# Performance work log

Measured on AMD Instinct MI355X. Metric: run time of the kernel, lower is better.

Reference implementation:

```python
import jax, jax.numpy as jnp
import numpy as np

EPS = 1e-5

def layernorm(x, w, b):
    mu = jnp.mean(x, axis=-1, keepdims=True)
    var = jnp.mean((x - mu) ** 2, axis=-1, keepdims=True)
    return (x - mu) / jnp.sqrt(var + EPS) * w + b

def setup_inputs() -> dict:
    key = jax.random.key(0)
    ks = jax.random.split(key, 20)
    N, E, G = 50000, 800000, 512
    IN, OUT, TXT, MAN = 128, 128, 768, 14
    d = {
        "x": jax.random.normal(ks[0], (N, IN), jnp.float32),
        "edge_index": jax.random.randint(ks[1], (2, E), 0, N),
        "batch": jnp.sort(jax.random.randint(ks[2], (N,), 0, G)),
        "batch_size": G,
        "text_embedding": jax.random.normal(ks[3], (G, TXT), jnp.float32),
        "features_embedding": jax.random.normal(ks[4], (G, MAN), jnp.float32),
        # params
        "ln_proj_w": jnp.ones((IN,)), "ln_proj_b": jnp.zeros((IN,)),
        "W_l": jax.random.normal(ks[5], (IN, OUT)) / np.sqrt(IN),
        "b_l": jnp.zeros((OUT,)),
        "W_r": jax.random.normal(ks[6], (IN, OUT)) / np.sqrt(IN),
        "ln_conv_w": jnp.ones((OUT,)), "ln_conv_b": jnp.zeros((OUT,)),
        "gate_w": jax.random.normal(ks[7], (OUT, 1)) / np.sqrt(OUT),
        "gate_b": jnp.zeros((1,)),
        "graph_weight": jnp.asarray(1.0, jnp.float32),
        "msg_W": jax.random.normal(ks[8], (TXT, OUT)) / np.sqrt(TXT),
        "msg_b": jnp.zeros((OUT,)),
        "feat_W": jax.random.normal(ks[9], (MAN, OUT)) / np.sqrt(MAN),
        "feat_b": jnp.zeros((OUT,)),
        "mixed_w": jnp.ones((3 * OUT,)), "mixed_b": jnp.zeros((3 * OUT,)),
        "fc1_W": jax.random.normal(ks[10], (3 * OUT, 1)) / np.sqrt(3 * OUT),
        "fc1_b": jnp.zeros((1,)),
    }
    return d

def reference(x, edge_index, batch, batch_size, text_embedding, features_embedding,
              ln_proj_w, ln_proj_b, W_l, b_l, W_r, ln_conv_w, ln_conv_b,
              gate_w, gate_b, graph_weight, msg_W, msg_b, feat_W, feat_b,
              mixed_w, mixed_b, fc1_W, fc1_b):
    N = x.shape[0]
    src, dst = edge_index[0], edge_index[1]
    # project_norm
    h = layernorm(x, ln_proj_w, ln_proj_b)
    # GraphSAGE (SAGEConv, mean aggregation): out = mean_j(h_j) @ W_l + b + h @ W_r
    msgs = h[src]                                   # [E, IN] gather
    agg = jax.ops.segment_sum(msgs, dst, num_segments=N)
    deg = jax.ops.segment_sum(jnp.ones((src.shape[0],), h.dtype), dst, num_segments=N)
    mean_nb = agg / jnp.maximum(deg, 1.0)[:, None]
    h = mean_nb @ W_l + b_l + h @ W_r
    # layernorm + gelu (HomogeneousGraphConvolution)
    h = jax.nn.gelu(layernorm(h, ln_conv_w, ln_conv_b), approximate=False)
    # AttentionalAggregation: scatter-softmax over `batch`
    gate = (h @ gate_w + gate_b)[:, 0]              # [N]
    seg_max = jax.ops.segment_max(gate, batch, num_segments=batch_size)
    seg_max = jnp.where(jnp.isfinite(seg_max), seg_max, 0.0)
    e = jnp.exp(gate - seg_max[batch])
    denom = jax.ops.segment_sum(e, batch, num_segments=batch_size)
    attn = (e / denom[batch])[:, None]              # [N,1]
    graph_embedding = jax.ops.segment_sum(attn * h, batch, num_segments=batch_size)
    # dropout is identity in eval mode
    weighted = graph_weight * graph_embedding
    msg_emb = jax.nn.gelu(text_embedding @ msg_W + msg_b, approximate=False)
    feat_emb = jax.nn.gelu(features_embedding @ feat_W + feat_b, approximate=False)
    emb = jnp.concatenate([weighted, msg_emb, feat_emb], axis=1)
    emb = layernorm(emb, mixed_w, mixed_b)
    logits = emb @ fc1_W + fc1_b
    return (logits, graph_embedding, attn)
```

## Files before the change

kernel.cpp:

```cpp
#include <hip/hip_runtime.h>


typedef unsigned short ushort_t;
typedef __attribute__((ext_vector_type(8))) short bf16x8;
typedef __attribute__((ext_vector_type(4))) float floatx4;

#define NBLK 128
#define MAXNB 1024

__device__ __forceinline__ float b2f(ushort_t u) {
    union { unsigned int i; float f; } v; v.i = ((unsigned int)u) << 16; return v.f;
}
__device__ __forceinline__ ushort_t f2b(float f) {
    union { float f; unsigned int i; } v; v.f = f;
    unsigned int x = v.i;
    return (ushort_t)((x + 0x7FFFu + ((x >> 16) & 1u)) >> 16);
}
__device__ __forceinline__ float gelu_f(float x) {
    return 0.5f * x * (1.0f + erff(x * 0.70710678118654752440f));
}
__device__ __forceinline__ float waveReduceSum(float v) {
#pragma unroll
    for (int o = 32; o; o >>= 1) v += __shfl_xor(v, o, 64);
    return v;
}
__device__ __forceinline__ float waveReduceMax(float v) {
#pragma unroll
    for (int o = 32; o; o >>= 1) v = fmaxf(v, __shfl_xor(v, o, 64));
    return v;
}
__device__ __forceinline__ int lowerBound(const int* __restrict__ a, int n, int v) {
    int lo = 0, hi = n;
    while (lo < hi) { int mid = (lo + hi) >> 1; if (a[mid] < v) lo = mid + 1; else hi = mid; }
    return lo;
}

__global__ void k_prep(const float* __restrict__ Wl, const float* __restrict__ Wr,
                       ushort_t* __restrict__ Wt) {
    int id = blockIdx.x * 256 + threadIdx.x;
    if (id >= 32768) return;
    int n = id >> 8, k = id & 255;
    float v = (k < 128) ? Wl[k * 128 + n] : Wr[(k - 128) * 128 + n];
    Wt[n * 256 + k] = f2b(v);
}

__global__ void k_ln1(const float* __restrict__ x, const float* __restrict__ w,
                      const float* __restrict__ b, ushort_t* __restrict__ hb, int N) {
    int row  = (blockIdx.x * blockDim.x + threadIdx.x) >> 6;
    int lane = threadIdx.x & 63;
    if (row >= N) return;
    size_t base = (size_t)row * 128;
    float2 xv = ((const float2*)(x + base))[lane];
    float v0 = xv.x, v1 = xv.y;
    float s  = waveReduceSum(v0 + v1);
    float s2 = waveReduceSum(v0 * v0 + v1 * v1);
    float mu = s * (1.0f / 128.0f);
    float var = s2 * (1.0f / 128.0f) - mu * mu;
    float rstd = 1.0f / sqrtf(var + 1e-5f);
    int d = lane * 2;
    ushort2 ov;
    ov.x = f2b((v0 - mu) * rstd * w[d]     + b[d]);
    ov.y = f2b((v1 - mu) * rstd * w[d + 1] + b[d + 1]);
    ((ushort2*)(hb + base))[lane] = ov;
}

__global__ void __launch_bounds__(256) k_deghist(
    const int* __restrict__ ei, int* __restrict__ deg, int* __restrict__ bhist,
    int E, int nb, int chunk) {
    __shared__ int hist[MAXNB];
    int blk = blockIdx.x, t = threadIdx.x;
    for (int i = t; i < nb; i += 256) hist[i] = 0;
    __syncthreads();
    int e0 = blk * chunk, e1 = min(e0 + chunk, E);
    for (int e = e0 + t; e < e1; e += 256) {
        int d = ei[E + e];
        atomicAdd(&deg[d], 1);
        atomicAdd(&hist[d >> 7], 1);
    }
    __syncthreads();
    for (int i = t; i < nb; i += 256) bhist[i * NBLK + blk] = hist[i];
}

__global__ void k_chunksum(const int* __restrict__ deg, int* __restrict__ csum, int N) {
    int i = blockIdx.x * 256 + threadIdx.x;
    int v = (i < N) ? deg[i] : 0;
#pragma unroll
    for (int o = 32; o; o >>= 1) v += __shfl_xor(v, o, 64);
    __shared__ int buf[4];
    int lane = threadIdx.x & 63, wv = threadIdx.x >> 6;
    if (lane == 0) buf[wv] = v;
    __syncthreads();
    if (threadIdx.x == 0) csum[blockIdx.x] = buf[0] + buf[1] + buf[2] + buf[3];
}
__global__ void k_chunkscan(const int* __restrict__ csum, int* __restrict__ coff, int nch) {
    int t = threadIdx.x;
    int v = (t < nch) ? csum[t] : 0;
    __shared__ int sb[256];
    sb[t] = v; __syncthreads();
    for (int o = 1; o < 256; o <<= 1) {
        int a = (t >= o) ? sb[t - o] : 0;
        __syncthreads();
        sb[t] += a;
        __syncthreads();
    }
    coff[t] = sb[t] - v;
}
__global__ void k_cursor(const int* __restrict__ deg, const int* __restrict__ coff,
                         int* __restrict__ cursor, int N) {
    int t = threadIdx.x;
    int i = blockIdx.x * 256 + t;
    int v = (i < N) ? deg[i] : 0;
    __shared__ int sb[256];
    sb[t] = v; __syncthreads();
    for (int o = 1; o < 256; o <<= 1) {
        int a = (t >= o) ? sb[t - o] : 0;
        __syncthreads();
        sb[t] += a;
        __syncthreads();
    }
    if (i < N) cursor[i] = sb[t] - v + coff[blockIdx.x];
}

__global__ void __launch_bounds__(256) k_bscan(
    const int* __restrict__ bhist, const int* __restrict__ cursor,
    int* __restrict__ boff, int nb) {
    int t = threadIdx.x;
    for (int b = t; b < nb; b += 256) {
        int run = cursor[b << 7];
        const int* row = bhist + b * NBLK;
#pragma unroll 8
        for (int blk = 0; blk < NBLK; blk++) {
            boff[blk * nb + b] = run;
            run += row[blk];
        }
    }
}

__global__ void __launch_bounds__(256) k_bplace(
    const int* __restrict__ ei, const int* __restrict__ boff,
    unsigned int* __restrict__ packed, int E, int nb, int chunk) {
    __shared__ int lcur[MAXNB];
    int blk = blockIdx.x, t = threadIdx.x;
    for (int i = t; i < nb; i += 256) lcur[i] = boff[blk * nb + i];
    __syncthreads();
    int e0 = blk * chunk, e1 = min(e0 + chunk, E);
    for (int e = e0 + t; e < e1; e += 256) {
        int s = ei[e], d = ei[E + e];
        int pos = atomicAdd(&lcur[d >> 7], 1);
        packed[pos] = ((unsigned int)(d & 127) << 25) | (unsigned int)s;
    }
}

__global__ void __launch_bounds__(256) k_bsort(
    const unsigned int* __restrict__ packed, const int* __restrict__ cursor,
    int* __restrict__ nbr, int N, int E) {
    __shared__ int lcur[128];
    int b = blockIdx.x, t = threadIdx.x;
    int node0 = b << 7;
    if (t < 128) {
        int node = node0 + t;
        lcur[t] = (node < N) ? cursor[node] : 0;
    }
    __syncthreads();
    int gstart = cursor[node0];
    int next = node0 + 128;
    int gend = (next < N) ? cursor[next] : E;
    for (int i = gstart + t; i < gend; i += 256) {
        unsigned int p = packed[i];
        int pos = atomicAdd(&lcur[p >> 25], 1);
        nbr[pos] = (int)(p & 0x1FFFFFFu);
    }
}

__global__ void k_aggcsr(const ushort_t* __restrict__ hb, const int* __restrict__ cursor,
                         const int* __restrict__ deg, const int* __restrict__ nbr,
                         ushort_t* __restrict__ meanb, int N) {
    int node = (blockIdx.x * blockDim.x + threadIdx.x) >> 6;
    int lane = threadIdx.x & 63;
    if (node >= N) return;
    int dg = deg[node];
    int st = cursor[node];
    float a0 = 0.f, a1 = 0.f;
    int j = 0;
    for (; j + 8 <= dg; j += 8) {
        int s0 = nbr[st + j],     s1 = nbr[st + j + 1];
        int s2 = nbr[st + j + 2], s3 = nbr[st + j + 3];
        int s4 = nbr[st + j + 4], s5 = nbr[st + j + 5];
        int s6 = nbr[st + j + 6], s7 = nbr[st + j + 7];
        ushort2 v0 = ((const ushort2*)(hb + (size_t)s0 * 128))[lane];
        ushort2 v1 = ((const ushort2*)(hb + (size_t)s1 * 128))[lane];
        ushort2 v2 = ((const ushort2*)(hb + (size_t)s2 * 128))[lane];
        ushort2 v3 = ((const ushort2*)(hb + (size_t)s3 * 128))[lane];
        ushort2 v4 = ((const ushort2*)(hb + (size_t)s4 * 128))[lane];
        ushort2 v5 = ((const ushort2*)(hb + (size_t)s5 * 128))[lane];
        ushort2 v6 = ((const ushort2*)(hb + (size_t)s6 * 128))[lane];
        ushort2 v7 = ((const ushort2*)(hb + (size_t)s7 * 128))[lane];
        a0 += b2f(v0.x) + b2f(v1.x) + b2f(v2.x) + b2f(v3.x)
            + b2f(v4.x) + b2f(v5.x) + b2f(v6.x) + b2f(v7.x);
        a1 += b2f(v0.y) + b2f(v1.y) + b2f(v2.y) + b2f(v3.y)
            + b2f(v4.y) + b2f(v5.y) + b2f(v6.y) + b2f(v7.y);
    }
    for (; j + 4 <= dg; j += 4) {
        int s0 = nbr[st + j],     s1 = nbr[st + j + 1];
        int s2 = nbr[st + j + 2], s3 = nbr[st + j + 3];
        ushort2 v0 = ((const ushort2*)(hb + (size_t)s0 * 128))[lane];
        ushort2 v1 = ((const ushort2*)(hb + (size_t)s1 * 128))[lane];
        ushort2 v2 = ((const ushort2*)(hb + (size_t)s2 * 128))[lane];
        ushort2 v3 = ((const ushort2*)(hb + (size_t)s3 * 128))[lane];
        a0 += b2f(v0.x) + b2f(v1.x) + b2f(v2.x) + b2f(v3.x);
        a1 += b2f(v0.y) + b2f(v1.y) + b2f(v2.y) + b2f(v3.y);
    }
    for (; j < dg; j++) {
        int s = nbr[st + j];
        ushort2 v = ((const ushort2*)(hb + (size_t)s * 128))[lane];
        a0 += b2f(v.x); a1 += b2f(v.y);
    }
    float inv = 1.0f / fmaxf((float)dg, 1.0f);
    ushort2 ov; ov.x = f2b(a0 * inv); ov.y = f2b(a1 * inv);
    ((ushort2*)(meanb + (size_t)node * 128))[lane] = ov;
}

__global__ void __launch_bounds__(256) k_gemm(
    const ushort_t* __restrict__ meanb, ushort_t* __restrict__ hb,
    const ushort_t* __restrict__ Wt, const float* __restrict__ bl,
    const float* __restrict__ lnw, const float* __restrict__ lnb,
    const float* __restrict__ gw, const float* __restrict__ gb,
    float* __restrict__ gate, int N) {
    __shared__ ushort_t A[16][264];
    __shared__ float H2[16][132];
    int t = threadIdx.x;
    int row0 = blockIdx.x * 16;
    {
        int r = t >> 4, i = t & 15;
        int row = row0 + r; if (row >= N) row = N - 1;
        *(bf16x8*)&A[r][i * 8]       = *(const bf16x8*)(meanb + (size_t)row * 128 + i * 8);
        *(bf16x8*)&A[r][128 + i * 8] = *(const bf16x8*)(hb    + (size_t)row * 128 + i * 8);
    }
    __syncthreads();
    int w = t >> 6, l = t & 63;
    int m16 = l & 15, quad = l >> 4;
    int n0 = w * 32 + m16;
    int n1 = n0 + 16;
    floatx4 acc0 = {0.f, 0.f, 0.f, 0.f}, acc1 = {0.f, 0.f, 0.f, 0.f};
    for (int ks = 0; ks < 256; ks += 32) {
        bf16x8 a  = *(const bf16x8*)&A[m16][ks + quad * 8];
        bf16x8 b0 = *(const bf16x8*)(Wt + (size_t)n0 * 256 + ks + quad * 8);
        bf16x8 b1 = *(const bf16x8*)(Wt + (size_t)n1 * 256 + ks + quad * 8);
        acc0 = __builtin_amdgcn_mfma_f32_16x16x32_bf16(a, b0, acc0, 0, 0, 0);
        acc1 = __builtin_amdgcn_mfma_f32_16x16x32_bf16(a, b1, acc1, 0, 0, 0);
    }
#pragma unroll
    for (int i = 0; i < 4; i++) {
        H2[quad * 4 + i][n0] = acc0[i];
        H2[quad * 4 + i][n1] = acc1[i];
    }
    __syncthreads();
    int d = l * 2;
    float bb0 = bl[d],  bb1 = bl[d + 1];
    float lw0 = lnw[d], lw1 = lnw[d + 1];
    float lb0 = lnb[d], lb1 = lnb[d + 1];
    float gw0 = gw[d],  gw1 = gw[d + 1];
    float gbias = gb[0];
#pragma unroll
    for (int rr = 0; rr < 4; rr++) {
        int r = w * 4 + rr;
        int row = row0 + r;
        if (row >= N) break;
        float v0 = H2[r][d] + bb0, v1 = H2[r][d + 1] + bb1;
        float s  = waveReduceSum(v0 + v1);
        float s2 = waveReduceSum(v0 * v0 + v1 * v1);
        float mu = s * (1.f / 128.f);
        float var = s2 * (1.f / 128.f) - mu * mu;
        float rstd = 1.0f / sqrtf(var + 1e-5f);
        float g0 = gelu_f((v0 - mu) * rstd * lw0 + lb0);
        float g1 = gelu_f((v1 - mu) * rstd * lw1 + lb1);
        float gp = waveReduceSum(g0 * gw0 + g1 * gw1);
        ushort2 ov; ov.x = f2b(g0); ov.y = f2b(g1);
        ((ushort2*)(hb + (size_t)row * 128))[l] = ov;
        if (l == 0) gate[row] = gp + gbias;
    }
}

__global__ void __launch_bounds__(128) k_attntail(
    const float* __restrict__ gate, const ushort_t* __restrict__ h3b,
    const int* __restrict__ batch,
    const float* __restrict__ text, const float* __restrict__ feats,
    const float* __restrict__ msgW, const float* __restrict__ msgb,
    const float* __restrict__ featW, const float* __restrict__ featb,
    const float* __restrict__ gwt, const float* __restrict__ mixw,
    const float* __restrict__ mixb, const float* __restrict__ fc1W,
    const float* __restrict__ fc1b,
    float* __restrict__ ge_out, float* __restrict__ attn_out,
    float* __restrict__ logits, int N, int G) {
    int g = blockIdx.x, t = threadIdx.x;
    __shared__ int sbound[2];
    __shared__ float wbuf[2];
    __shared__ float pbuf[128];
    __shared__ float txt[768];
    __shared__ float rbuf[4];
    if (t < 2) sbound[t] = lowerBound(batch, N, g + t);
    for (int i = t; i < 768; i += 128) txt[i] = text[(size_t)g * 768 + i];
    __syncthreads();
    int s0 = sbound[0], s1 = sbound[1];
    int lane = t & 63, wv = t >> 6;
    float acc = 0.f;
    if (s1 > s0) {
        float m = -3.0e38f;
        for (int i = s0 + t; i < s1; i += 128) m = fmaxf(m, gate[i]);
        m = waveReduceMax(m);
        if (lane == 0) wbuf[wv] = m;
        __syncthreads();
        m = fmaxf(wbuf[0], wbuf[1]);
        __syncthreads();
        float dsum = 0.f;
        for (int i = s0 + t; i < s1; i += 128) dsum += expf(gate[i] - m);
        dsum = waveReduceSum(dsum);
        if (lane == 0) wbuf[wv] = dsum;
        __syncthreads();
        float inv = 1.0f / (wbuf[0] + wbuf[1]);
        for (int base = s0; base < s1; base += 128) {
            int n = min(128, s1 - base);
            __syncthreads();
            if (t < n) {
                float p = expf(gate[base + t] - m) * inv;
                pbuf[t] = p;
                attn_out[base + t] = p;
            }
            __syncthreads();
            for (int j = 0; j < n; j++)
                acc += pbuf[j] * b2f(h3b[(size_t)(base + j) * 128 + t]);
        }
    }
    ge_out[(size_t)g * 128 + t] = acc;
    float am = msgb[t];
    for (int k = 0; k < 768; k += 4) {
        float4 a = *(const float4*)&txt[k];
        am += a.x * msgW[(k + 0) * 128 + t] + a.y * msgW[(k + 1) * 128 + t]
            + a.z * msgW[(k + 2) * 128 + t] + a.w * msgW[(k + 3) * 128 + t];
    }
    float me = gelu_f(am);
    float af = featb[t];
#pragma unroll
    for (int k = 0; k < 14; k++) af += feats[g * 14 + k] * featW[k * 128 + t];
    float fe = gelu_f(af);
    float e0 = gwt[0] * acc;
    float ps = e0 + me + fe, ps2 = e0 * e0 + me * me + fe * fe;
    float r1 = waveReduceSum(ps), r2 = waveReduceSum(ps2);
    __syncthreads();
    if (lane == 0) { rbuf[wv] = r1; rbuf[2 + wv] = r2; }
    __syncthreads();
    float S = rbuf[0] + rbuf[1], S2 = rbuf[2] + rbuf[3];
    float mu = S * (1.f / 384.f);
    float var = S2 * (1.f / 384.f) - mu * mu;
    float rstd = 1.0f / sqrtf(var + 1e-5f);
    float n0 = (e0 - mu) * rstd * mixw[t]       + mixb[t];
    float n1 = (me - mu) * rstd * mixw[128 + t] + mixb[128 + t];
    float n2 = (fe - mu) * rstd * mixw[256 + t] + mixb[256 + t];
    float lp = n0 * fc1W[t] + n1 * fc1W[128 + t] + n2 * fc1W[256 + t];
    float r3 = waveReduceSum(lp);
    __syncthreads();
    if (lane == 0) rbuf[wv] = r3;
    __syncthreads();
    if (t == 0) logits[g] = rbuf[0] + rbuf[1] + fc1b[0];
}

extern "C" void kernel_launch(void* const* d_in, const int* in_sizes, int n_in,
                              void* d_out, int out_size, void* d_ws, size_t ws_size,
                              hipStream_t stream) {
    const float* x     = (const float*)d_in[0];
    const int*   ei    = (const int*)d_in[1];
    const int*   batch = (const int*)d_in[2];
    const float* text  = (const float*)d_in[4];
    const float* feats = (const float*)d_in[5];
    const float* lnpw  = (const float*)d_in[6];
    const float* lnpb  = (const float*)d_in[7];
    const float* Wl    = (const float*)d_in[8];
    const float* bl    = (const float*)d_in[9];
    const float* Wr    = (const float*)d_in[10];
    const float* lncw  = (const float*)d_in[11];
    const float* lncb  = (const float*)d_in[12];
    const float* gatew = (const float*)d_in[13];
    const float* gateb = (const float*)d_in[14];
    const float* gwt   = (const float*)d_in[15];
    const float* msgW  = (const float*)d_in[16];
    const float* msgb  = (const float*)d_in[17];
    const float* featW = (const float*)d_in[18];
    const float* featb = (const float*)d_in[19];
    const float* mixw  = (const float*)d_in[20];
    const float* mixb  = (const float*)d_in[21];
    const float* fc1W  = (const float*)d_in[22];
    const float* fc1b  = (const float*)d_in[23];

    int N = in_sizes[0] / 128;
    int E = in_sizes[1] / 2;
    int G = in_sizes[4] / 768;

    char* wp = (char*)d_ws;
    auto alloc = [&](size_t bytes) -> char* {
        char* p = wp; wp += (bytes + 255) & ~(size_t)255; return p;
    };
    ushort_t* hb     = (ushort_t*)alloc((size_t)N * 128 * 2);
    ushort_t* meanb  = (ushort_t*)alloc((size_t)N * 128 * 2);
    ushort_t* Wt     = (ushort_t*)alloc(128 * 256 * 2);
    float*    gate   = (float*)alloc((size_t)N * 4);
    int*      deg    = (int*)alloc((size_t)N * 4);
    int*      cursor = (int*)alloc((size_t)N * 4);
    int*      nbr    = (int*)alloc((size_t)E * 4);
    unsigned int* packed = (unsigned int*)alloc((size_t)E * 4);
    int*      csum   = (int*)alloc(1024 * 4);
    int*      coff   = (int*)alloc(1024 * 4);

    int nch = (N + 255) / 256;
    int nb  = (N + 127) / 128;
    int chunk = (E + NBLK - 1) / NBLK;

    int* bhist = (int*)alloc((size_t)nb * NBLK * 4);
    int* boff  = (int*)alloc((size_t)NBLK * nb * 4);

    float* logits_out = (float*)d_out;
    float* ge_out     = logits_out + G;
    float* attn_out   = ge_out + (size_t)G * 128;

    hipMemsetAsync(deg, 0, (size_t)N * 4, stream);

    k_prep     <<<128,               256, 0, stream>>>(Wl, Wr, Wt);
    k_ln1      <<<(N + 3) / 4,       256, 0, stream>>>(x, lnpw, lnpb, hb, N);
    k_deghist  <<<NBLK,              256, 0, stream>>>(ei, deg, bhist, E, nb, chunk);
    k_chunksum <<<nch,               256, 0, stream>>>(deg, csum, N);
    k_chunkscan<<<1,                 256, 0, stream>>>(csum, coff, nch);
    k_cursor   <<<nch,               256, 0, stream>>>(deg, coff, cursor, N);
    k_bscan    <<<1,                 256, 0, stream>>>(bhist, cursor, boff, nb);
    k_bplace   <<<NBLK,              256, 0, stream>>>(ei, boff, packed, E, nb, chunk);
    k_bsort    <<<nb,                256, 0, stream>>>(packed, cursor, nbr, N, E);
    k_aggcsr   <<<(N + 3) / 4,       256, 0, stream>>>(hb, cursor, deg, nbr, meanb, N);
    k_gemm     <<<(N + 15) / 16,     256, 0, stream>>>(meanb, hb, Wt, bl, lncw, lncb,
                                                       gatew, gateb, gate, N);
    k_attntail <<<G,                 128, 0, stream>>>(gate, hb, batch, text, feats,
                                                       msgW, msgb, featW, featb, gwt,
                                                       mixw, mixb, fc1W, fc1b,
                                                       ge_out, attn_out, logits_out, N, G);
}
```

Baseline: 294.3 us.

## Fuse neighbor aggregation into GEMM and merge prep, layernorm and scan kernels

Fuses the CSR mean-aggregation into the GEMM kernel, so each block gathers neighbor rows with 16-byte loads, four neighbors at a time per wave, and writes the mean straight into shared memory instead of a global meanb buffer. The GEMM output goes to a separate h3b buffer so hb stays readable by other blocks. Weight prep, degree zeroing and the first layernorm are merged into one launch. The three-kernel degree scan plus the bucket-offset scan become a single 1024-thread block. This cuts launches and the meanb round trip, at the cost of serial single-block scanning and per-node shuffle reductions inside the GEMM kernel.

```diff
diff --git a/kernel.cpp b/kernel.cpp
--- a/kernel.cpp
+++ b/kernel.cpp
@@ -35,18 +35,24 @@
     return lo;
 }
 
-__global__ void k_prep(const float* __restrict__ Wl, const float* __restrict__ Wr,
-                       ushort_t* __restrict__ Wt) {
-    int id = blockIdx.x * 256 + threadIdx.x;
-    if (id >= 32768) return;
-    int n = id >> 8, k = id & 255;
-    float v = (k < 128) ? Wl[k * 128 + n] : Wr[(k - 128) * 128 + n];
-    Wt[n * 256 + k] = f2b(v);
-}
-
-__global__ void k_ln1(const float* __restrict__ x, const float* __restrict__ w,
-                      const float* __restrict__ b, ushort_t* __restrict__ hb, int N) {
-    int row  = (blockIdx.x * blockDim.x + threadIdx.x) >> 6;
+__global__ void __launch_bounds__(256) k_prepln(
+    const float* __restrict__ x, const float* __restrict__ w, const float* __restrict__ b,
+    const float* __restrict__ Wl, const float* __restrict__ Wr,
+    ushort_t* __restrict__ Wt, ushort_t* __restrict__ hb, int* __restrict__ deg, int N) {
+    int bid = blockIdx.x;
+    if (bid < 128) {
+        int id = bid * 256 + threadIdx.x;
+        int n = id >> 8, k = id & 255;
+        float v = (k < 128) ? Wl[k * 128 + n] : Wr[(k - 128) * 128 + n];
+        Wt[n * 256 + k] = f2b(v);
+        return;
+    }
+    int lb = bid - 128;
+    if (threadIdx.x < 4) {
+        int rz = lb * 4 + threadIdx.x;
+        if (rz < N) deg[rz] = 0;
+    }
+    int row  = lb * 4 + (threadIdx.x >> 6);
     int lane = threadIdx.x & 63;
     if (row >= N) return;
     size_t base = (size_t)row * 128;
@@ -81,57 +87,39 @@
     for (int i = t; i < nb; i += 256) bhist[i * NBLK + blk] = hist[i];
 }
 
-__global__ void k_chunksum(const int* __restrict__ deg, int* __restrict__ csum, int N) {
-    int i = blockIdx.x * 256 + threadIdx.x;
-    int v = (i < N) ? deg[i] : 0;
-#pragma unroll
-    for (int o = 32; o; o >>= 1) v += __shfl_xor(v, o, 64);
-    __shared__ int buf[4];
-    int lane = threadIdx.x & 63, wv = threadIdx.x >> 6;
-    if (lane == 0) buf[wv] = v;
-    __syncthreads();
-    if (threadIdx.x == 0) csum[blockIdx.x] = buf[0] + buf[1] + buf[2] + buf[3];
-}
-__global__ void k_chunkscan(const int* __restrict__ csum, int* __restrict__ coff, int nch) {
+__global__ void __launch_bounds__(1024) k_scanboff(
+    const int* __restrict__ deg, int* __restrict__ cursor,
+    const int* __restrict__ bhist, int* __restrict__ boff, int N, int nb) {
+    __shared__ int sb[1024];
     int t = threadIdx.x;
-    int v = (t < nch) ? csum[t] : 0;
-    __shared__ int sb[256];
-    sb[t] = v; __syncthreads();
-    for (int o = 1; o < 256; o <<= 1) {
+    int per = (N + 1023) >> 10;
+    int base = t * per;
+    int s = 0;
+    for (int i = 0; i < per; i++) {
+        int idx = base + i;
+        if (idx < N) s += deg[idx];
+    }
+    sb[t] = s;
+    __syncthreads();
+    for (int o = 1; o < 1024; o <<= 1) {
         int a = (t >= o) ? sb[t - o] : 0;
         __syncthreads();
         sb[t] += a;
         __syncthreads();
     }
-    coff[t] = sb[t] - v;
-}
-__global__ void k_cursor(const int* __restrict__ deg, const int* __restrict__ coff,
-                         int* __restrict__ cursor, int N) {
-    int t = threadIdx.x;
-    int i = blockIdx.x * 256 + t;
-    int v = (i < N) ? deg[i] : 0;
-    __shared__ int sb[256];
-    sb[t] = v; __syncthreads();
-    for (int o = 1; o < 256; o <<= 1) {
-        int a = (t >= o) ? sb[t - o] : 0;
-        __syncthreads();
-        sb[t] += a;
-        __syncthreads();
-    }
-    if (i < N) cursor[i] = sb[t] - v + coff[blockIdx.x];
-}
-
-__global__ void __launch_bounds__(256) k_bscan(
-    const int* __restrict__ bhist, const int* __restrict__ cursor,
-    int* __restrict__ boff, int nb) {
-    int t = threadIdx.x;
-    for (int b = t; b < nb; b += 256) {
-        int run = cursor[b << 7];
-        const int* row = bhist + b * NBLK;
+    int run = sb[t] - s;
+    for (int i = 0; i < per; i++) {
+        int idx = base + i;
+        if (idx < N) { cursor[idx] = run; run += deg[idx]; }
+    }
+    __syncthreads();
+    for (int bkt = t; bkt < nb; bkt += 1024) {
+        int run2 = cursor[bkt << 7];
+        const int* row = bhist + bkt * NBLK;
 #pragma unroll 8
         for (int blk = 0; blk < NBLK; blk++) {
-            boff[blk * nb + b] = run;
-            run += row[blk];
+            boff[blk * nb + bkt] = run2;
+            run2 += row[blk];
         }
     }
 }
@@ -172,72 +160,70 @@
     }
 }
 
-__global__ void k_aggcsr(const ushort_t* __restrict__ hb, const int* __restrict__ cursor,
-                         const int* __restrict__ deg, const int* __restrict__ nbr,
-                         ushort_t* __restrict__ meanb, int N) {
-    int node = (blockIdx.x * blockDim.x + threadIdx.x) >> 6;
-    int lane = threadIdx.x & 63;
-    if (node >= N) return;
-    int dg = deg[node];
-    int st = cursor[node];
-    float a0 = 0.f, a1 = 0.f;
-    int j = 0;
-    for (; j + 8 <= dg; j += 8) {
-        int s0 = nbr[st + j],     s1 = nbr[st + j + 1];
-        int s2 = nbr[st + j + 2], s3 = nbr[st + j + 3];
-        int s4 = nbr[st + j + 4], s5 = nbr[st + j + 5];
-        int s6 = nbr[st + j + 6], s7 = nbr[st + j + 7];
-        ushort2 v0 = ((const ushort2*)(hb + (size_t)s0 * 128))[lane];
-        ushort2 v1 = ((const ushort2*)(hb + (size_t)s1 * 128))[lane];
-        ushort2 v2 = ((const ushort2*)(hb + (size_t)s2 * 128))[lane];
-        ushort2 v3 = ((const ushort2*)(hb + (size_t)s3 * 128))[lane];
-        ushort2 v4 = ((const ushort2*)(hb + (size_t)s4 * 128))[lane];
-        ushort2 v5 = ((const ushort2*)(hb + (size_t)s5 * 128))[lane];
-        ushort2 v6 = ((const ushort2*)(hb + (size_t)s6 * 128))[lane];
-        ushort2 v7 = ((const ushort2*)(hb + (size_t)s7 * 128))[lane];
-        a0 += b2f(v0.x) + b2f(v1.x) + b2f(v2.x) + b2f(v3.x)
-            + b2f(v4.x) + b2f(v5.x) + b2f(v6.x) + b2f(v7.x);
-        a1 += b2f(v0.y) + b2f(v1.y) + b2f(v2.y) + b2f(v3.y)
-            + b2f(v4.y) + b2f(v5.y) + b2f(v6.y) + b2f(v7.y);
-    }
-    for (; j + 4 <= dg; j += 4) {
-        int s0 = nbr[st + j],     s1 = nbr[st + j + 1];
-        int s2 = nbr[st + j + 2], s3 = nbr[st + j + 3];
-        ushort2 v0 = ((const ushort2*)(hb + (size_t)s0 * 128))[lane];
-        ushort2 v1 = ((const ushort2*)(hb + (size_t)s1 * 128))[lane];
-        ushort2 v2 = ((const ushort2*)(hb + (size_t)s2 * 128))[lane];
-        ushort2 v3 = ((const ushort2*)(hb + (size_t)s3 * 128))[lane];
-        a0 += b2f(v0.x) + b2f(v1.x) + b2f(v2.x) + b2f(v3.x);
-        a1 += b2f(v0.y) + b2f(v1.y) + b2f(v2.y) + b2f(v3.y);
-    }
-    for (; j < dg; j++) {
-        int s = nbr[st + j];
-        ushort2 v = ((const ushort2*)(hb + (size_t)s * 128))[lane];
-        a0 += b2f(v.x); a1 += b2f(v.y);
-    }
-    float inv = 1.0f / fmaxf((float)dg, 1.0f);
-    ushort2 ov; ov.x = f2b(a0 * inv); ov.y = f2b(a1 * inv);
-    ((ushort2*)(meanb + (size_t)node * 128))[lane] = ov;
-}
-
-__global__ void __launch_bounds__(256) k_gemm(
-    const ushort_t* __restrict__ meanb, ushort_t* __restrict__ hb,
-    const ushort_t* __restrict__ Wt, const float* __restrict__ bl,
-    const float* __restrict__ lnw, const float* __restrict__ lnb,
-    const float* __restrict__ gw, const float* __restrict__ gb,
-    float* __restrict__ gate, int N) {
+__global__ void __launch_bounds__(256) k_aggemm(
+    const ushort_t* __restrict__ hb, const ushort_t* __restrict__ Wt,
+    const float* __restrict__ bl, const float* __restrict__ lnw,
+    const float* __restrict__ lnb, const float* __restrict__ gw,
+    const float* __restrict__ gb, const int* __restrict__ deg,
+    const int* __restrict__ cursor, const int* __restrict__ nbr,
+    ushort_t* __restrict__ h3b, float* __restrict__ gate, int N) {
     __shared__ ushort_t A[16][264];
     __shared__ float H2[16][132];
     int t = threadIdx.x;
     int row0 = blockIdx.x * 16;
-    {
-        int r = t >> 4, i = t & 15;
-        int row = row0 + r; if (row >= N) row = N - 1;
-        *(bf16x8*)&A[r][i * 8]       = *(const bf16x8*)(meanb + (size_t)row * 128 + i * 8);
-        *(bf16x8*)&A[r][128 + i * 8] = *(const bf16x8*)(hb    + (size_t)row * 128 + i * 8);
-    }
-    __syncthreads();
     int w = t >> 6, l = t & 63;
+    int sub = l >> 4, li = l & 15;
+    for (int rr = 0; rr < 4; rr++) {
+        int r = w * 4 + rr;
+        int node = row0 + r; if (node >= N) node = N - 1;
+        if (sub == 2) {
+            bf16x8 hv = *(const bf16x8*)(hb + (size_t)node * 128 + li * 8);
+            *(bf16x8*)&A[r][128 + li * 8] = hv;
+        }
+        int dg = deg[node];
+        int st = cursor[node];
+        float a0 = 0.f, a1 = 0.f, a2 = 0.f, a3 = 0.f;
+        float a4 = 0.f, a5 = 0.f, a6 = 0.f, a7 = 0.f;
+        for (int j = 0; j < dg; j += 8) {
+            int i0 = j + sub, i1 = j + 4 + sub;
+            bf16x8 r0 = {0,0,0,0,0,0,0,0};
+            bf16x8 r1 = {0,0,0,0,0,0,0,0};
+            if (i0 < dg) {
+                int s = nbr[st + i0];
+                r0 = *(const bf16x8*)(hb + (size_t)s * 128 + li * 8);
+            }
+            if (i1 < dg) {
+                int s = nbr[st + i1];
+                r1 = *(const bf16x8*)(hb + (size_t)s * 128 + li * 8);
+            }
+            a0 += b2f((ushort_t)r0[0]) + b2f((ushort_t)r1[0]);
+            a1 += b2f((ushort_t)r0[1]) + b2f((ushort_t)r1[1]);
+            a2 += b2f((ushort_t)r0[2]) + b2f((ushort_t)r1[2]);
+            a3 += b2f((ushort_t)r0[3]) + b2f((ushort_t)r1[3]);
+            a4 += b2f((ushort_t)r0[4]) + b2f((ushort_t)r1[4]);
+            a5 += b2f((ushort_t)r0[5]) + b2f((ushort_t)r1[5]);
+            a6 += b2f((ushort_t)r0[6]) + b2f((ushort_t)r1[6]);
+            a7 += b2f((ushort_t)r0[7]) + b2f((ushort_t)r1[7]);
+        }
+        a0 += __shfl_xor(a0, 16, 64); a0 += __shfl_xor(a0, 32, 64);
+        a1 += __shfl_xor(a1, 16, 64); a1 += __shfl_xor(a1, 32, 64);
+        a2 += __shfl_xor(a2, 16, 64); a2 += __shfl_xor(a2, 32, 64);
+        a3 += __shfl_xor(a3, 16, 64); a3 += __shfl_xor(a3, 32, 64);
+        a4 += __shfl_xor(a4, 16, 64); a4 += __shfl_xor(a4, 32, 64);
+        a5 += __shfl_xor(a5, 16, 64); a5 += __shfl_xor(a5, 32, 64);
+        a6 += __shfl_xor(a6, 16, 64); a6 += __shfl_xor(a6, 32, 64);
+        a7 += __shfl_xor(a7, 16, 64); a7 += __shfl_xor(a7, 32, 64);
+        if (sub == 0) {
+            float inv = 1.0f / fmaxf((float)dg, 1.0f);
+            bf16x8 ov;
+            ov[0] = (short)f2b(a0 * inv); ov[1] = (short)f2b(a1 * inv);
+            ov[2] = (short)f2b(a2 * inv); ov[3] = (short)f2b(a3 * inv);
+            ov[4] = (short)f2b(a4 * inv); ov[5] = (short)f2b(a5 * inv);
+            ov[6] = (short)f2b(a6 * inv); ov[7] = (short)f2b(a7 * inv);
+            *(bf16x8*)&A[r][li * 8] = ov;
+        }
+    }
+    __syncthreads();
     int m16 = l & 15, quad = l >> 4;
     int n0 = w * 32 + m16;
     int n1 = n0 + 16;
@@ -276,7 +262,7 @@
         float g1 = gelu_f((v1 - mu) * rstd * lw1 + lb1);
         float gp = waveReduceSum(g0 * gw0 + g1 * gw1);
         ushort2 ov; ov.x = f2b(g0); ov.y = f2b(g1);
-        ((ushort2*)(hb + (size_t)row * 128))[l] = ov;
+        ((ushort2*)(h3b + (size_t)row * 128))[l] = ov;
         if (l == 0) gate[row] = gp + gbias;
     }
 }
@@ -400,17 +386,14 @@
         char* p = wp; wp += (bytes + 255) & ~(size_t)255; return p;
     };
     ushort_t* hb     = (ushort_t*)alloc((size_t)N * 128 * 2);
-    ushort_t* meanb  = (ushort_t*)alloc((size_t)N * 128 * 2);
+    ushort_t* h3b    = (ushort_t*)alloc((size_t)N * 128 * 2);
     ushort_t* Wt     = (ushort_t*)alloc(128 * 256 * 2);
     float*    gate   = (float*)alloc((size_t)N * 4);
     int*      deg    = (int*)alloc((size_t)N * 4);
     int*      cursor = (int*)alloc((size_t)N * 4);
     int*      nbr    = (int*)alloc((size_t)E * 4);
     unsigned int* packed = (unsigned int*)alloc((size_t)E * 4);
-    int*      csum   = (int*)alloc(1024 * 4);
-    int*      coff   = (int*)alloc(1024 * 4);
-
-    int nch = (N + 255) / 256;
+
     int nb  = (N + 127) / 128;
     int chunk = (E + NBLK - 1) / NBLK;
 
@@ -421,21 +404,14 @@
     float* ge_out     = logits_out + G;
     float* attn_out   = ge_out + (size_t)G * 128;
 
-    hipMemsetAsync(deg, 0, (size_t)N * 4, stream);
-
-    k_prep     <<<128,               256, 0, stream>>>(Wl, Wr, Wt);
-    k_ln1      <<<(N + 3) / 4,       256, 0, stream>>>(x, lnpw, lnpb, hb, N);
+    k_prepln   <<<128 + (N + 3) / 4, 256, 0, stream>>>(x, lnpw, lnpb, Wl, Wr, Wt, hb, deg, N);
     k_deghist  <<<NBLK,              256, 0, stream>>>(ei, deg, bhist, E, nb, chunk);
-    k_chunksum <<<nch,               256, 0, stream>>>(deg, csum, N);
-    k_chunkscan<<<1,                 256, 0, stream>>>(csum, coff, nch);
-    k_cursor   <<<nch,               256, 0, stream>>>(deg, coff, cursor, N);
-    k_bscan    <<<1,                 256, 0, stream>>>(bhist, cursor, boff, nb);
+    k_scanboff <<<1,                1024, 0, stream>>>(deg, cursor, bhist, boff, N, nb);
     k_bplace   <<<NBLK,              256, 0, stream>>>(ei, boff, packed, E, nb, chunk);
     k_bsort    <<<nb,                256, 0, stream>>>(packed, cursor, nbr, N, E);
-    k_aggcsr   <<<(N + 3) / 4,       256, 0, stream>>>(hb, cursor, deg, nbr, meanb, N);
-    k_gemm     <<<(N + 15) / 16,     256, 0, stream>>>(meanb, hb, Wt, bl, lncw, lncb,
-                                                       gatew, gateb, gate, N);
-    k_attntail <<<G,                 128, 0, stream>>>(gate, hb, batch, text, feats,
+    k_aggemm   <<<(N + 15) / 16,     256, 0, stream>>>(hb, Wt, bl, lncw, lncb, gatew, gateb,
+                                                       deg, cursor, nbr, h3b, gate, N);
+    k_attntail <<<G,                 128, 0, stream>>>(gate, h3b, batch, text, feats,
                                                        msgW, msgb, featW, featb, gwt,
                                                        mixw, mixb, fc1W, fc1b,
                                                        ge_out, attn_out, logits_out, N, G);
```

Measured after the change: 372.2 us. 1.26x slower.
